# Kernel tuning notes

Hardware: AMD Instinct MI355X
Metric: run time of the kernel (lower is better)

The kernel has to match this reference:

```python
import jax, jax.numpy as jnp
import numpy as np

NUM_HEADS = 8


def setup_inputs() -> dict:
    key = jax.random.key(0)
    k1, k2, k3 = jax.random.split(key, 3)
    B, N, C = 4, 2048, 1024
    x = jax.random.normal(k1, (B, N, C), dtype=jnp.float32)
    # torch nn.Linear layout: [out_features, in_features]; scaled for stability
    Wqkv = jax.random.normal(k2, (3 * C, C), dtype=jnp.float32) * (C ** -0.5)
    Wproj = jax.random.normal(k3, (C, C), dtype=jnp.float32) * (C ** -0.5)
    return {"x": x, "Wqkv": Wqkv, "Wproj": Wproj}


def reference(x, Wqkv, Wproj):
    B, N, C = x.shape
    H = NUM_HEADS
    D = C // H
    # fused QKV projection (bias=False per config)
    qkv = jnp.einsum('bnc,oc->bno', x, Wqkv)          # [B, N, 3C]
    qkv = qkv.reshape(B, N, 3, H, D)
    q = jnp.transpose(qkv[:, :, 0], (0, 2, 1, 3))     # [B, H, N, D]
    k = jnp.transpose(qkv[:, :, 1], (0, 2, 1, 3))
    v = jnp.transpose(qkv[:, :, 2], (0, 2, 1, 3))
    scale = 1.0 / jnp.sqrt(jnp.asarray(D, dtype=x.dtype))
    scores = jnp.einsum('bhqd,bhkd->bhqk', q, k) * scale
    attn = jax.nn.softmax(scores, axis=-1)            # attn_drop is identity (p=0)
    out = jnp.einsum('bhqk,bhkd->bhqd', attn, v)      # [B, H, N, D]
    out = jnp.transpose(out, (0, 2, 1, 3)).reshape(B, N, C)
    out = jnp.einsum('bnc,oc->bno', out, Wproj)       # proj_drop is identity (p=0)
    return out
```

## Files before the change

### kernel.cpp

```cpp
#include <hip/hip_runtime.h>
#include <hip/hip_bf16.h>
#include <stdint.h>


typedef __bf16 bf16x8 __attribute__((ext_vector_type(8)));
typedef float  f32x4  __attribute__((ext_vector_type(4)));
typedef float  f32x16 __attribute__((ext_vector_type(16)));
typedef short  s16x8  __attribute__((ext_vector_type(8)));
typedef unsigned int u32x4 __attribute__((ext_vector_type(4)));

__device__ __forceinline__ f32x4 mfma_bf16(s16x8 a, s16x8 b, f32x4 c) {
  return __builtin_amdgcn_mfma_f32_16x16x32_bf16(
      __builtin_bit_cast(bf16x8, a), __builtin_bit_cast(bf16x8, b), c, 0, 0, 0);
}

__device__ __forceinline__ f32x16 mfma32(s16x8 a, s16x8 b, f32x16 c) {
  return __builtin_amdgcn_mfma_f32_32x32x16_bf16(
      __builtin_bit_cast(bf16x8, a), __builtin_bit_cast(bf16x8, b), c, 0, 0, 0);
}

__device__ __forceinline__ unsigned short f2bf(float f) {
  unsigned u = __float_as_uint(f);
  u = u + 0x7FFFu + ((u >> 16) & 1u);
  return (unsigned short)(u >> 16);
}

__device__ __forceinline__ unsigned cvt_pk_bf16(float lo, float hi) {
  unsigned r;
  asm("v_cvt_pk_bf16_f32 %0, %1, %2" : "=v"(r) : "v"(lo), "v"(hi));
  return r;
}

__device__ __forceinline__ void load_lds16(const void* g, void* l) {
  __builtin_amdgcn_global_load_lds(
      (const __attribute__((address_space(1))) void*)g,
      (__attribute__((address_space(3))) void*)l, 16, 0, 0);
}


__global__ void cast3_kernel(const float* __restrict__ x, const float* __restrict__ wq,
                             const float* __restrict__ wp,
                             unsigned short* __restrict__ xb,
                             unsigned short* __restrict__ wqb,
                             unsigned short* __restrict__ wpb) {
  int i = blockIdx.x * blockDim.x + threadIdx.x;
  int stride = gridDim.x * blockDim.x;
  for (; i < 3145728; i += stride) {
    const float4* src; ushort4* dst; int j;
    if (i < 2097152)      { src = (const float4*)x;  dst = (ushort4*)xb;  j = i; }
    else if (i < 2883584) { src = (const float4*)wq; dst = (ushort4*)wqb; j = i - 2097152; }
    else                  { src = (const float4*)wp; dst = (ushort4*)wpb; j = i - 2883584; }
    float4 v = src[j];
    ushort4 o;
    o.x = f2bf(v.x); o.y = f2bf(v.y); o.z = f2bf(v.z); o.w = f2bf(v.w);
    dst[j] = o;
  }
}


template <bool OUT_BF16>
__global__ __launch_bounds__(512, 2)
void gemm256(const short* __restrict__ A, const short* __restrict__ Bw,
             void* __restrict__ Cp, int M, int N, int K) {
  __shared__ __align__(16) short a_lds[2][256 * 64];
  __shared__ __align__(16) short b_lds[2][256 * 64];

  const int nbn = N >> 8;
  const int nwg = gridDim.x;
  const int q8 = nwg >> 3;
  const int swz = (blockIdx.x & 7) * q8 + (blockIdx.x >> 3);
  const int mb = swz / nbn, nb = swz % nbn;

  const int tid = threadIdx.x;
  const int w = tid >> 6, l = tid & 63;
  const int lg = l >> 4, ll = l & 15;
  const int wm = w >> 2, wn = w & 3;

  f32x4 acc[8][4];
#pragma unroll
  for (int i = 0; i < 8; ++i)
#pragma unroll
    for (int j = 0; j < 4; ++j) acc[i][j] = {0.f, 0.f, 0.f, 0.f};

  const int NT = K >> 6;

  auto stage = [&](int t, int g) {
    short* lptr = (g < 2) ? b_lds[t & 1] : a_lds[t & 1];
    const short* gp = (g < 2) ? Bw : A;
    const int gg = g & 1;
#pragma unroll
    for (int j = 0; j < 2; ++j) {
      int r0 = gg * 128 + w * 16 + j * 8;
      int rl = r0 + (l >> 3);
      int grow;
      if (g < 2) grow = nb * 256 + rl;
      else       grow = mb * 256 + ((rl >> 6) & 1) * 128 + (rl >> 7) * 64 + (rl & 63);
      const short* src = gp + (size_t)grow * K + t * 64 + (((l & 7) ^ (l >> 3)) << 3);
      load_lds16(src, lptr + r0 * 64);
    }
  };

#define GQ_PHASE(QM, KK, GG, ...)                                              \
  {                                                                            \
    const short* ab = a_lds[cur];                                              \
    const short* bb = b_lds[cur];                                              \
    const int slot = (((KK) * 4 + lg) ^ (ll & 7)) * 8;                         \
    s16x8 af[4], bfr[4];                                                       \
    _Pragma("unroll") for (int mi = 0; mi < 4; ++mi)                           \
      af[mi] = *reinterpret_cast<const s16x8*>(                                \
          ab + ((QM) * 128 + wm * 64 + mi * 16 + ll) * 64 + slot);             \
    _Pragma("unroll") for (int nj = 0; nj < 4; ++nj)                           \
      bfr[nj] = *reinterpret_cast<const s16x8*>(                               \
          bb + (wn * 64 + nj * 16 + ll) * 64 + slot);                          \
    if (pf) stage(t + 1, (GG));                                                \
    __builtin_amdgcn_s_barrier();                                              \
    asm volatile("s_waitcnt lgkmcnt(0)" ::: "memory");                         \
    __builtin_amdgcn_sched_barrier(0);                                         \
    __builtin_amdgcn_s_setprio(1);                                             \
    _Pragma("unroll") for (int mi = 0; mi < 4; ++mi)                           \
      _Pragma("unroll") for (int nj = 0; nj < 4; ++nj)                         \
        acc[(QM) * 4 + mi][nj] = mfma_bf16(af[mi], bfr[nj], acc[(QM) * 4 + mi][nj]); \
    __builtin_amdgcn_s_setprio(0);                                             \
    __VA_ARGS__                                                                \
    __builtin_amdgcn_s_barrier();                                              \
  }

  stage(0, 0); stage(0, 1); stage(0, 2); stage(0, 3);
  asm volatile("s_waitcnt vmcnt(2)" ::: "memory");
  __builtin_amdgcn_s_barrier();

  for (int t = 0; t < NT; ++t) {
    const int cur = t & 1;
    const bool pf = (t + 1 < NT);
    GQ_PHASE(0, 0, 0, )
    GQ_PHASE(0, 1, 1,
      if (pf) { asm volatile("s_waitcnt vmcnt(4)" ::: "memory"); }
      else    { asm volatile("s_waitcnt vmcnt(0)" ::: "memory"); })
    GQ_PHASE(1, 0, 2, )
    GQ_PHASE(1, 1, 3,
      if (pf) { asm volatile("s_waitcnt vmcnt(2)" ::: "memory"); }
      else    { asm volatile("s_waitcnt vmcnt(0)" ::: "memory"); })
  }
#undef GQ_PHASE

#pragma unroll
  for (int qm = 0; qm < 2; ++qm)
#pragma unroll
    for (int mi = 0; mi < 4; ++mi)
#pragma unroll
      for (int i = 0; i < 4; ++i) {
        size_t row = (size_t)(mb * 256 + wm * 128 + qm * 64 + mi * 16 + lg * 4 + i);
#pragma unroll
        for (int nj = 0; nj < 4; ++nj) {
          int col = nb * 256 + wn * 64 + nj * 16 + ll;
          if (OUT_BF16)
            ((unsigned short*)Cp)[row * N + col] = f2bf(acc[qm * 4 + mi][nj][i]);
          else
            ((float*)Cp)[row * N + col] = acc[qm * 4 + mi][nj][i];
        }
      }
}


__global__ __launch_bounds__(512, 2)
void attn_fwd(const short* __restrict__ qkv, unsigned short* __restrict__ aout) {
  __shared__ __align__(16) short k_lds[2][64 * 128];
  __shared__ __align__(16) short v_lds[2][128 * 64];

  const int bh = blockIdx.x >> 3;
  const int qb = blockIdx.x & 7;
  const int b = bh >> 3, h = bh & 7;
  const int tid = threadIdx.x;
  const int w = tid >> 6, l = tid & 63;
  const int col = l & 31, hi = l >> 5;

  const size_t base = (size_t)b * 2048 * 3072 + (size_t)h * 128;
  const int qrow0 = qb * 256 + w * 32;

  s16x8 qf[8];
  {
    const short* qp = qkv + base + (size_t)(qrow0 + col) * 3072 + hi * 8;
#pragma unroll
    for (int ks = 0; ks < 8; ++ks)
      qf[ks] = *reinterpret_cast<const s16x8*>(qp + ks * 16);
  }

  f32x16 oacc[4];
#pragma unroll
  for (int nt = 0; nt < 4; ++nt)
#pragma unroll
    for (int r = 0; r < 16; ++r) oacc[nt][r] = 0.f;
  float M = -1e30f, L = 0.f;
  const float csc = 0.08838834764831845f * 1.4426950408889634f;

  s16x8 vr0a, vr0b, vr1a, vr1b;
  const int vr_r0 = (tid & 31) * 2;
  const int vr_c0 = ((tid >> 5) & 7) * 16;

  auto stage_k = [&](int kb, int bf) {
    int wk = w - 4;
#pragma unroll
    for (int cc = 0; cc < 4; ++cc) {
      int c = wk * 4 + cc;
      int row = c * 4 + (l >> 4);
      int sd = (l & 15) ^ (row & 7);
      load_lds16(qkv + base + 1024 + (size_t)(kb * 64 + row) * 3072 + sd * 8,
                 &k_lds[bf][c * 512]);
    }
  };
  auto load_v = [&](int kb) {
    const short* g = qkv + base + 2048 + (size_t)(kb * 64 + vr_r0) * 3072 + vr_c0;
    vr0a = *reinterpret_cast<const s16x8*>(g);
    vr0b = *reinterpret_cast<const s16x8*>(g + 8);
    vr1a = *reinterpret_cast<const s16x8*>(g + 3072);
    vr1b = *reinterpret_cast<const s16x8*>(g + 3072 + 8);
  };
  auto write_v = [&](int bf) {
    char* vbase = reinterpret_cast<char*>(v_lds[bf]);
#pragma unroll
    for (int j = 0; j < 16; ++j) {
      int d = vr_c0 + j;
      unsigned e0 = (unsigned short)(j < 8 ? vr0a[j] : vr0b[j - 8]);
      unsigned e1 = (unsigned short)(j < 8 ? vr1a[j] : vr1b[j - 8]);
      int byte = d * 128 + ((((vr_r0 * 2) >> 4) ^ (d & 7)) << 4) + ((vr_r0 * 2) & 15);
      *reinterpret_cast<unsigned*>(vbase + byte) = e0 | (e1 << 16);
    }
  };

  if (w >= 4) stage_k(0, 0);
  else { load_v(0); write_v(0); }
  __syncthreads();

  for (int kb = 0; kb < 32; ++kb) {
    const int bf = kb & 1;
    if (kb < 31) {
      if (w >= 4) stage_k(kb + 1, bf ^ 1);
      else load_v(kb + 1);
    }

    f32x16 st[2];
#pragma unroll
    for (int kt = 0; kt < 2; ++kt)
#pragma unroll
      for (int r = 0; r < 16; ++r) st[kt][r] = 0.f;
    const char* kbase = reinterpret_cast<const char*>(k_lds[bf]);
    __builtin_amdgcn_s_setprio(1);
#pragma unroll
    for (int ks = 0; ks < 8; ++ks) {
#pragma unroll
      for (int kt = 0; kt < 2; ++kt) {
        int krow = kt * 32 + col;
        int slot = (ks * 2 + hi) ^ (krow & 7);
        s16x8 ak = *reinterpret_cast<const s16x8*>(kbase + krow * 256 + slot * 16);
        st[kt] = mfma32(ak, qf[ks], st[kt]);
      }
    }
    __builtin_amdgcn_s_setprio(0);

    float pm = st[0][0];
#pragma unroll
    for (int r = 1; r < 16; ++r) pm = fmaxf(pm, st[0][r]);
#pragma unroll
    for (int r = 0; r < 16; ++r) pm = fmaxf(pm, st[1][r]);
    pm *= csc;
    pm = fmaxf(pm, __shfl_xor(pm, 32));
    if (!__all(pm <= M + 8.0f)) {
      float Mn = fmaxf(M, pm);
      float f = exp2f(M - Mn);
      M = Mn; L *= f;
#pragma unroll
      for (int r = 0; r < 16; ++r) {
        float fr = __shfl(f, (r & 3) + 8 * (r >> 2) + 4 * hi);
#pragma unroll
        for (int nt = 0; nt < 4; ++nt) oacc[nt][r] *= fr;
      }
    }
    float rs = 0.f;
#pragma unroll
    for (int kt = 0; kt < 2; ++kt)
#pragma unroll
      for (int r = 0; r < 16; ++r) {
        float e = exp2f(fmaf(st[kt][r], csc, -M));
        st[kt][r] = e;
        rs += e;
      }
    rs += __shfl_xor(rs, 32);
    L += rs;

    unsigned wd[16], pw[16];
#pragma unroll
    for (int i = 0; i < 8; ++i) {
      wd[i]     = cvt_pk_bf16(st[0][2 * i], st[0][2 * i + 1]);
      wd[8 + i] = cvt_pk_bf16(st[1][2 * i], st[1][2 * i + 1]);
    }
#pragma unroll
    for (int i = 0; i < 16; ++i) pw[i] = __shfl_xor(wd[i], 32);
    s16x8 pa[4];
#pragma unroll
    for (int kt = 0; kt < 2; ++kt) {
      int bq = kt * 8;
      u32x4 f0 = {hi ? pw[bq + 2] : wd[bq + 0], hi ? pw[bq + 3] : wd[bq + 1],
                  hi ? wd[bq + 2] : pw[bq + 0], hi ? wd[bq + 3] : pw[bq + 1]};
      u32x4 f1 = {hi ? pw[bq + 6] : wd[bq + 4], hi ? pw[bq + 7] : wd[bq + 5],
                  hi ? wd[bq + 6] : pw[bq + 4], hi ? wd[bq + 7] : pw[bq + 5]};
      pa[kt * 2 + 0] = __builtin_bit_cast(s16x8, f0);
      pa[kt * 2 + 1] = __builtin_bit_cast(s16x8, f1);
    }

    const char* vbase = reinterpret_cast<const char*>(v_lds[bf]);
    __builtin_amdgcn_s_setprio(1);
#pragma unroll
    for (int ks = 0; ks < 4; ++ks) {
#pragma unroll
      for (int nt = 0; nt < 4; ++nt) {
        int d = nt * 32 + col;
        int slot = (ks * 2 + hi) ^ (d & 7);
        s16x8 bv = *reinterpret_cast<const s16x8*>(vbase + d * 128 + slot * 16);
        oacc[nt] = mfma32(pa[ks], bv, oacc[nt]);
      }
    }
    __builtin_amdgcn_s_setprio(0);

    if (kb < 31 && w < 4) write_v(bf ^ 1);
    __syncthreads();
  }

  float invl = 1.f / L;
#pragma unroll
  for (int r = 0; r < 16; ++r) {
    int qr = (r & 3) + 8 * (r >> 2) + 4 * hi;
    float il = __shfl(invl, qr);
    size_t row = (size_t)b * 2048 + qrow0 + qr;
#pragma unroll
    for (int nt = 0; nt < 4; ++nt)
      aout[row * 1024 + h * 128 + nt * 32 + col] = f2bf(oacc[nt][r] * il);
  }
}


extern "C" void kernel_launch(void* const* d_in, const int* in_sizes, int n_in,
                              void* d_out, int out_size, void* d_ws, size_t ws_size,
                              hipStream_t stream) {
  const float* x     = (const float*)d_in[0];
  const float* wqkv  = (const float*)d_in[1];
  const float* wproj = (const float*)d_in[2];
  float* out = (float*)d_out;

  char* ws = (char*)d_ws;
  short* xb     = (short*)(ws);
  short* wqkvb  = (short*)(ws + 16777216);
  short* wprojb = (short*)(ws + 23068672);
  short* qkvb   = (short*)(ws + 25165824);
  short* aoutb  = (short*)(ws + 75497472);

  cast3_kernel<<<2048, 256, 0, stream>>>(x, wqkv, wproj,
      (unsigned short*)xb, (unsigned short*)wqkvb, (unsigned short*)wprojb);

  gemm256<true><<<384, 512, 0, stream>>>(xb, wqkvb, (void*)qkvb, 8192, 3072, 1024);

  attn_fwd<<<32 * 8, 512, 0, stream>>>(qkvb, (unsigned short*)aoutb);

  gemm256<false><<<128, 512, 0, stream>>>(aoutb, wprojb, (void*)out, 8192, 1024, 1024);
}
```

Measured before the change: 285.4 us.

## Head-major QKV layout, software-pipelined PV, B-fragment reuse, higher attention occupancy

The QKV GEMM epilogue now writes Q, K and V into separate head-major planes, so attention loads are contiguous 256-byte rows instead of strided by 3072. The GEMM phase order is changed to reuse the B fragments across two M halves, which removes half the B LDS reads. The attention loop defers the PV matmul of the previous block to overlap with the next QK^T, adds a tree max reduction, and raises launch bounds to 4 blocks. The new barrier structure and the higher occupancy target risk register pressure or spills.

```diff
diff --git a/kernel.cpp b/kernel.cpp
--- a/kernel.cpp
+++ b/kernel.cpp
@@ -100,18 +100,21 @@
     }
   };
 
-#define GQ_PHASE(QM, KK, GG, ...)                                              \
+  s16x8 af[4], bfr[4];
+
+#define GQ_PHASE(QM, KK, RB, GG, ...)                                          \
   {                                                                            \
     const short* ab = a_lds[cur];                                              \
     const short* bb = b_lds[cur];                                              \
     const int slot = (((KK) * 4 + lg) ^ (ll & 7)) * 8;                         \
-    s16x8 af[4], bfr[4];                                                       \
     _Pragma("unroll") for (int mi = 0; mi < 4; ++mi)                           \
       af[mi] = *reinterpret_cast<const s16x8*>(                                \
           ab + ((QM) * 128 + wm * 64 + mi * 16 + ll) * 64 + slot);             \
-    _Pragma("unroll") for (int nj = 0; nj < 4; ++nj)                           \
-      bfr[nj] = *reinterpret_cast<const s16x8*>(                               \
-          bb + (wn * 64 + nj * 16 + ll) * 64 + slot);                          \
+    if (RB) {                                                                  \
+      _Pragma("unroll") for (int nj = 0; nj < 4; ++nj)                         \
+        bfr[nj] = *reinterpret_cast<const s16x8*>(                             \
+            bb + (wn * 64 + nj * 16 + ll) * 64 + slot);                        \
+    }                                                                          \
     if (pf) stage(t + 1, (GG));                                                \
     __builtin_amdgcn_s_barrier();                                              \
     asm volatile("s_waitcnt lgkmcnt(0)" ::: "memory");                         \
@@ -132,14 +135,14 @@
   for (int t = 0; t < NT; ++t) {
     const int cur = t & 1;
     const bool pf = (t + 1 < NT);
-    GQ_PHASE(0, 0, 0, )
-    GQ_PHASE(0, 1, 1,
-      if (pf) { asm volatile("s_waitcnt vmcnt(4)" ::: "memory"); }
-      else    { asm volatile("s_waitcnt vmcnt(0)" ::: "memory"); })
-    GQ_PHASE(1, 0, 2, )
-    GQ_PHASE(1, 1, 3,
+    GQ_PHASE(0, 0, 1, 0,
       if (pf) { asm volatile("s_waitcnt vmcnt(2)" ::: "memory"); }
       else    { asm volatile("s_waitcnt vmcnt(0)" ::: "memory"); })
+    GQ_PHASE(1, 0, 0, 1, )
+    GQ_PHASE(0, 1, 1, 2, )
+    GQ_PHASE(1, 1, 0, 3,
+      if (pf) { asm volatile("s_waitcnt vmcnt(2)" ::: "memory"); }
+      else    { asm volatile("s_waitcnt vmcnt(0)" ::: "memory"); })
   }
 #undef GQ_PHASE
 
@@ -149,20 +152,30 @@
     for (int mi = 0; mi < 4; ++mi)
 #pragma unroll
       for (int i = 0; i < 4; ++i) {
-        size_t row = (size_t)(mb * 256 + wm * 128 + qm * 64 + mi * 16 + lg * 4 + i);
-#pragma unroll
-        for (int nj = 0; nj < 4; ++nj) {
-          int col = nb * 256 + wn * 64 + nj * 16 + ll;
-          if (OUT_BF16)
-            ((unsigned short*)Cp)[row * N + col] = f2bf(acc[qm * 4 + mi][nj][i]);
-          else
-            ((float*)Cp)[row * N + col] = acc[qm * 4 + mi][nj][i];
+        int row = mb * 256 + wm * 128 + qm * 64 + mi * 16 + lg * 4 + i;
+        if (OUT_BF16) {
+          int bb2 = row >> 11, n = row & 2047;
+          size_t rbase = (size_t)(bb2 * 8) * 262144 + (size_t)n * 128;
+#pragma unroll
+          for (int nj = 0; nj < 4; ++nj) {
+            int colb = nb * 256 + wn * 64 + nj * 16;
+            int pl = colb >> 10, hh = (colb >> 7) & 7, dd = colb & 127;
+            ((unsigned short*)Cp)[(size_t)pl * 8388608 + rbase +
+                                  (size_t)hh * 262144 + dd + ll] =
+                f2bf(acc[qm * 4 + mi][nj][i]);
+          }
+        } else {
+#pragma unroll
+          for (int nj = 0; nj < 4; ++nj) {
+            int col = nb * 256 + wn * 64 + nj * 16 + ll;
+            ((float*)Cp)[(size_t)row * N + col] = acc[qm * 4 + mi][nj][i];
+          }
         }
       }
 }
 
 
-__global__ __launch_bounds__(512, 2)
+__global__ __launch_bounds__(512, 4)
 void attn_fwd(const short* __restrict__ qkv, unsigned short* __restrict__ aout) {
   __shared__ __align__(16) short k_lds[2][64 * 128];
   __shared__ __align__(16) short v_lds[2][128 * 64];
@@ -174,12 +187,15 @@
   const int w = tid >> 6, l = tid & 63;
   const int col = l & 31, hi = l >> 5;
 
-  const size_t base = (size_t)b * 2048 * 3072 + (size_t)h * 128;
+  const size_t plane = (size_t)32 * 2048 * 128;
+  const short* Qp = qkv + (size_t)(b * 8 + h) * 2048 * 128;
+  const short* Kp = Qp + plane;
+  const short* Vp = Qp + 2 * plane;
   const int qrow0 = qb * 256 + w * 32;
 
   s16x8 qf[8];
   {
-    const short* qp = qkv + base + (size_t)(qrow0 + col) * 3072 + hi * 8;
+    const short* qp = Qp + (size_t)(qrow0 + col) * 128 + hi * 8;
 #pragma unroll
     for (int ks = 0; ks < 8; ++ks)
       qf[ks] = *reinterpret_cast<const s16x8*>(qp + ks * 16);
@@ -204,16 +220,15 @@
       int c = wk * 4 + cc;
       int row = c * 4 + (l >> 4);
       int sd = (l & 15) ^ (row & 7);
-      load_lds16(qkv + base + 1024 + (size_t)(kb * 64 + row) * 3072 + sd * 8,
-                 &k_lds[bf][c * 512]);
+      load_lds16(Kp + (size_t)(kb * 64 + row) * 128 + sd * 8, &k_lds[bf][c * 512]);
     }
   };
   auto load_v = [&](int kb) {
-    const short* g = qkv + base + 2048 + (size_t)(kb * 64 + vr_r0) * 3072 + vr_c0;
+    const short* g = Vp + (size_t)(kb * 64 + vr_r0) * 128 + vr_c0;
     vr0a = *reinterpret_cast<const s16x8*>(g);
     vr0b = *reinterpret_cast<const s16x8*>(g + 8);
-    vr1a = *reinterpret_cast<const s16x8*>(g + 3072);
-    vr1b = *reinterpret_cast<const s16x8*>(g + 3072 + 8);
+    vr1a = *reinterpret_cast<const s16x8*>(g + 128);
+    vr1b = *reinterpret_cast<const s16x8*>(g + 128 + 8);
   };
   auto write_v = [&](int bf) {
     char* vbase = reinterpret_cast<char*>(v_lds[bf]);
@@ -227,6 +242,21 @@
     }
   };
 
+  s16x8 pa[4];
+  auto do_pv = [&](int vb) {
+    const char* vbase = reinterpret_cast<const char*>(v_lds[vb]);
+#pragma unroll
+    for (int ks = 0; ks < 4; ++ks) {
+#pragma unroll
+      for (int nt = 0; nt < 4; ++nt) {
+        int d = nt * 32 + col;
+        int slot = (ks * 2 + hi) ^ (d & 7);
+        s16x8 bv = *reinterpret_cast<const s16x8*>(vbase + d * 128 + slot * 16);
+        oacc[nt] = mfma32(pa[ks], bv, oacc[nt]);
+      }
+    }
+  };
+
   if (w >= 4) stage_k(0, 0);
   else { load_v(0); write_v(0); }
   __syncthreads();
@@ -238,13 +268,15 @@
       else load_v(kb + 1);
     }
 
+    __builtin_amdgcn_s_setprio(1);
+    if (kb > 0) do_pv(bf ^ 1);
+
     f32x16 st[2];
 #pragma unroll
     for (int kt = 0; kt < 2; ++kt)
 #pragma unroll
       for (int r = 0; r < 16; ++r) st[kt][r] = 0.f;
     const char* kbase = reinterpret_cast<const char*>(k_lds[bf]);
-    __builtin_amdgcn_s_setprio(1);
 #pragma unroll
     for (int ks = 0; ks < 8; ++ks) {
 #pragma unroll
@@ -257,12 +289,14 @@
     }
     __builtin_amdgcn_s_setprio(0);
 
-    float pm = st[0][0];
-#pragma unroll
-    for (int r = 1; r < 16; ++r) pm = fmaxf(pm, st[0][r]);
-#pragma unroll
-    for (int r = 0; r < 16; ++r) pm = fmaxf(pm, st[1][r]);
-    pm *= csc;
+    float t16[16];
+#pragma unroll
+    for (int r = 0; r < 16; ++r) t16[r] = fmaxf(st[0][r], st[1][r]);
+#pragma unroll
+    for (int s = 8; s >= 1; s >>= 1)
+#pragma unroll
+      for (int r = 0; r < s; ++r) t16[r] = fmaxf(t16[r], t16[r + s]);
+    float pm = t16[0] * csc;
     pm = fmaxf(pm, __shfl_xor(pm, 32));
     if (!__all(pm <= M + 8.0f)) {
       float Mn = fmaxf(M, pm);
@@ -295,7 +329,6 @@
     }
 #pragma unroll
     for (int i = 0; i < 16; ++i) pw[i] = __shfl_xor(wd[i], 32);
-    s16x8 pa[4];
 #pragma unroll
     for (int kt = 0; kt < 2; ++kt) {
       int bq = kt * 8;
@@ -307,23 +340,13 @@
       pa[kt * 2 + 1] = __builtin_bit_cast(s16x8, f1);
     }
 
-    const char* vbase = reinterpret_cast<const char*>(v_lds[bf]);
-    __builtin_amdgcn_s_setprio(1);
-#pragma unroll
-    for (int ks = 0; ks < 4; ++ks) {
-#pragma unroll
-      for (int nt = 0; nt < 4; ++nt) {
-        int d = nt * 32 + col;
-        int slot = (ks * 2 + hi) ^ (d & 7);
-        s16x8 bv = *reinterpret_cast<const s16x8*>(vbase + d * 128 + slot * 16);
-        oacc[nt] = mfma32(pa[ks], bv, oacc[nt]);
-      }
-    }
-    __builtin_amdgcn_s_setprio(0);
-
+    __builtin_amdgcn_s_barrier();
     if (kb < 31 && w < 4) write_v(bf ^ 1);
-    __syncthreads();
-  }
+    asm volatile("s_waitcnt vmcnt(0) lgkmcnt(0)" ::: "memory");
+    __builtin_amdgcn_s_barrier();
+  }
+
+  do_pv(1);
 
   float invl = 1.f / L;
 #pragma unroll
```

New measurement: 480.4 us. 1.68x slower.
